# Kernel optimization log

Measured on AMD Instinct MI355X. Metric: run time of the kernel, lower is better.

The kernel has to match this reference:

```python
import jax, jax.numpy as jnp
import numpy as np
from jax.scipy.linalg import expm

DIM = 2048        # state dimension (init arg `dim`)
M_STEPS = 8192    # kernel length (init arg `timestamp`)
DELTA = 0.01      # ZOH step size (init arg `delta`)
STAB = 1e-3       # stabilizer added to A before inversion (matches torch code)


def setup_inputs() -> dict:
    key = jax.random.key(0)
    k1, k2, k3 = jax.random.split(key, 3)
    # Match the torch init scaling so matrix_exp/inv stay well-conditioned.
    A = jnp.eye(DIM, dtype=jnp.float32) * -0.01 \
        + jax.random.normal(k1, (DIM, DIM), dtype=jnp.float32) * 0.001
    B = jax.random.normal(k2, (DIM, 1), dtype=jnp.float32) * 0.01
    C = jax.random.normal(k3, (1, DIM), dtype=jnp.float32) * 0.01
    return {"A": A, "B": B, "C": C, "M": M_STEPS}


def reference(A, B, C, M):
    dim = A.shape[0]
    I = jnp.eye(dim, dtype=A.dtype)
    # --- ZOH discretization (torch._zoh_discretize) ---
    A_bar = expm(DELTA * A)                         # [dim, dim]
    A_inv = jnp.linalg.inv(A + STAB * I)            # [dim, dim]
    B_bar = A_inv @ (A_bar - I) @ (DELTA * B)       # [dim, 1]

    # --- kernel power iteration (torch._compute_K_bar) ---
    # K[t] = C @ A_bar^t @ B_bar. Since B_bar is a vector, the serial
    # matrix-power loop reduces to M sequential matvecs (same math).
    def step(x, _):
        term = (C @ x)[0, 0]        # scalar K_t
        return A_bar @ x, term      # advance state: A_bar^{t+1} B_bar

    _, terms = jax.lax.scan(step, B_bar, None, length=M)  # [M]
    K_bar = terms[::-1][None, :]    # flip along time, shape [1, M]
    return K_bar
```

## Files before the change

kernel.cpp:

```cpp
#include <hip/hip_runtime.h>
#include <hip/hip_bf16.h>


#define DIMN 2048
#define MSTEPS 8192
#define RSPLIT 91
#define NN ((size_t)DIMN * DIMN)
#define NBLK 32
#define ALD 36
#define GJP 65

typedef short short8 __attribute__((ext_vector_type(8)));
typedef float f32x4 __attribute__((ext_vector_type(4)));

__device__ inline void split1(float x, unsigned short& h, unsigned short& l)
{
  __hip_bfloat16 b = __float2bfloat16(x);
  h = *reinterpret_cast<unsigned short*>(&b);
  float r = x - __bfloat162float(b);
  __hip_bfloat16 b2 = __float2bfloat16(r);
  l = *reinterpret_cast<unsigned short*>(&b2);
}

__global__ __launch_bounds__(256)
void k_combine4(float* out,
                const float* i1, float c1, const float* i2, float c2,
                const float* i3, float c3, const float* i4, float c4,
                float dval)
{
  const int total = DIMN * DIMN;
  for (int idx = blockIdx.x * 256 + threadIdx.x; idx < total; idx += gridDim.x * 256) {
    float v = 0.f;
    if (i1) v = fmaf(c1, i1[idx], v);
    if (i2) v = fmaf(c2, i2[idx], v);
    if (i3) v = fmaf(c3, i3[idx], v);
    if (i4) v = fmaf(c4, i4[idx], v);
    if ((idx >> 11) == (idx & 2047)) v += dval;
    out[idx] = v;
  }
}

__global__ __launch_bounds__(256)
void k_fill64(const float* __restrict__ A, double* __restrict__ M)
{
  const int total = DIMN * DIMN;
  for (int idx = blockIdx.x * 256 + threadIdx.x; idx < total; idx += gridDim.x * 256) {
    double v = (double)A[idx];
    if ((idx >> 11) == (idx & 2047)) v += 1e-3;
    M[idx] = v;
  }
}

__global__ __launch_bounds__(256)
void k_split(const float* __restrict__ in, unsigned short* __restrict__ hi,
             unsigned short* __restrict__ lo)
{
  const int i4 = blockIdx.x * 256 + threadIdx.x;
  const float4 v = ((const float4*)in)[i4];
  ushort4 h, l;
  split1(v.x, h.x, l.x); split1(v.y, h.y, l.y);
  split1(v.z, h.z, l.z); split1(v.w, h.w, l.w);
  ((ushort4*)hi)[i4] = h;
  ((ushort4*)lo)[i4] = l;
}

__global__ __launch_bounds__(256)
void k_splitT(const float* __restrict__ in, unsigned short* __restrict__ hi,
              unsigned short* __restrict__ lo)
{
  __shared__ float t[32][33];
  const int bx = blockIdx.x * 32, by = blockIdx.y * 32;
  const int lx = threadIdx.x, ly = threadIdx.y;
  for (int dy = 0; dy < 32; dy += 8)
    t[ly + dy][lx] = in[(size_t)(by + ly + dy) * DIMN + bx + lx];
  __syncthreads();
  for (int dy = 0; dy < 32; dy += 8) {
    const size_t o = (size_t)(bx + ly + dy) * DIMN + by + lx;
    unsigned short h, l;
    split1(t[lx][ly + dy], h, l);
    hi[o] = h; lo[o] = l;
  }
}

__global__ __launch_bounds__(256)
void k_gemm3(const unsigned short* __restrict__ Ahg, const unsigned short* __restrict__ Alg,
             const unsigned short* __restrict__ Bhg, const unsigned short* __restrict__ Blg,
             float* __restrict__ C, float alpha,
             const float* E1, float c1, const float* E2, float c2)
{
  __shared__ unsigned short sAh[128 * ALD];
  __shared__ unsigned short sAl[128 * ALD];
  __shared__ unsigned short sBh[128 * ALD];
  __shared__ unsigned short sBl[128 * ALD];
  const int tid = threadIdx.x;
  const int wid = tid >> 6, lane = tid & 63;
  const int lr = lane & 15, lg = lane >> 4;
  const int wm = wid >> 1, wn = wid & 1;
  const int brow = blockIdx.y * 128, bcol = blockIdx.x * 128;
  const int sr = tid >> 1, sh = (tid & 1) * 16;

  const unsigned short* gAh = Ahg + (size_t)(brow + sr) * DIMN + sh;
  const unsigned short* gAl = Alg + (size_t)(brow + sr) * DIMN + sh;
  const unsigned short* gBh = Bhg + (size_t)(bcol + sr) * DIMN + sh;
  const unsigned short* gBl = Blg + (size_t)(bcol + sr) * DIMN + sh;

  f32x4 acc[4][4];
#pragma unroll
  for (int mf = 0; mf < 4; ++mf)
#pragma unroll
    for (int nf = 0; nf < 4; ++nf) acc[mf][nf] = (f32x4){0.f, 0.f, 0.f, 0.f};

  uint4 pa0 = *(const uint4*)gAh;      uint4 pa1 = *(const uint4*)(gAh + 8);
  uint4 pb0 = *(const uint4*)gAl;      uint4 pb1 = *(const uint4*)(gAl + 8);
  uint4 pc0 = *(const uint4*)gBh;      uint4 pc1 = *(const uint4*)(gBh + 8);
  uint4 pd0 = *(const uint4*)gBl;      uint4 pd1 = *(const uint4*)(gBl + 8);

  const int nk = DIMN / 32;
  for (int kt = 0; kt < nk; ++kt) {
    *(uint4*)&sAh[sr * ALD + sh] = pa0;  *(uint4*)&sAh[sr * ALD + sh + 8] = pa1;
    *(uint4*)&sAl[sr * ALD + sh] = pb0;  *(uint4*)&sAl[sr * ALD + sh + 8] = pb1;
    *(uint4*)&sBh[sr * ALD + sh] = pc0;  *(uint4*)&sBh[sr * ALD + sh + 8] = pc1;
    *(uint4*)&sBl[sr * ALD + sh] = pd0;  *(uint4*)&sBl[sr * ALD + sh + 8] = pd1;
    __syncthreads();
    if (kt + 1 < nk) {
      const int o = (kt + 1) * 32;
      pa0 = *(const uint4*)(gAh + o);  pa1 = *(const uint4*)(gAh + o + 8);
      pb0 = *(const uint4*)(gAl + o);  pb1 = *(const uint4*)(gAl + o + 8);
      pc0 = *(const uint4*)(gBh + o);  pc1 = *(const uint4*)(gBh + o + 8);
      pd0 = *(const uint4*)(gBl + o);  pd1 = *(const uint4*)(gBl + o + 8);
    }
    short8 bh[4], bl[4];
#pragma unroll
    for (int nf = 0; nf < 4; ++nf) {
      const int br = 64 * wn + 16 * nf + lr;
      bh[nf] = *(const short8*)&sBh[br * ALD + lg * 8];
      bl[nf] = *(const short8*)&sBl[br * ALD + lg * 8];
    }
#pragma unroll
    for (int mf = 0; mf < 4; ++mf) {
      const int ar = 64 * wm + 16 * mf + lr;
      const short8 ah = *(const short8*)&sAh[ar * ALD + lg * 8];
      const short8 al = *(const short8*)&sAl[ar * ALD + lg * 8];
#pragma unroll
      for (int nf = 0; nf < 4; ++nf) {
        acc[mf][nf] = __builtin_amdgcn_mfma_f32_16x16x32_bf16(ah, bh[nf], acc[mf][nf], 0, 0, 0);
        acc[mf][nf] = __builtin_amdgcn_mfma_f32_16x16x32_bf16(ah, bl[nf], acc[mf][nf], 0, 0, 0);
        acc[mf][nf] = __builtin_amdgcn_mfma_f32_16x16x32_bf16(al, bh[nf], acc[mf][nf], 0, 0, 0);
      }
    }
    __syncthreads();
  }
#pragma unroll
  for (int mf = 0; mf < 4; ++mf) {
#pragma unroll
    for (int nf = 0; nf < 4; ++nf) {
      const int col = bcol + 64 * wn + 16 * nf + lr;
#pragma unroll
      for (int i = 0; i < 4; ++i) {
        const int row = brow + 64 * wm + 16 * mf + 4 * lg + i;
        float v = alpha * acc[mf][nf][i];
        if (E1) v = fmaf(c1, E1[(size_t)row * DIMN + col], v);
        if (E2) v = fmaf(c2, E2[(size_t)row * DIMN + col], v);
        C[(size_t)row * DIMN + col] = v;
      }
    }
  }
}

#define DBM 64
#define DBK 8
__global__ __launch_bounds__(256)
void k_dgemm(const double* __restrict__ A, int lda,
             const double* __restrict__ B, int ldb,
             double* C, int ldc, int K, double alpha,
             const double* E1, int ld1, double c1)
{
  __shared__ double As[DBK][DBM];
  __shared__ double Bs[DBK][DBM];
  const int tid = threadIdx.x;
  const int tx = tid & 15, ty = tid >> 4;
  const int brow = blockIdx.y * DBM, bcol = blockIdx.x * DBM;

  const int arow = tid >> 2, ac0 = (tid & 3) * 2;
  const int brw  = tid >> 5, bc0 = (tid & 31) * 2;

  const double* Aptr = A + (size_t)(brow + arow) * lda + ac0;
  const double* Bptr = B + (size_t)brw * ldb + (bcol + bc0);

  double2 aPre = *(const double2*)Aptr;
  double2 bPre = *(const double2*)Bptr;

  double acc[4][4];
#pragma unroll
  for (int i = 0; i < 4; ++i)
#pragma unroll
    for (int j = 0; j < 4; ++j) acc[i][j] = 0.0;

  const int nk = K / DBK;
  for (int kt = 0; kt < nk; ++kt) {
    As[ac0 + 0][arow] = aPre.x;
    As[ac0 + 1][arow] = aPre.y;
    Bs[brw][bc0 + 0] = bPre.x;
    Bs[brw][bc0 + 1] = bPre.y;
    __syncthreads();
    if (kt + 1 < nk) {
      aPre = *(const double2*)(Aptr + (size_t)(kt + 1) * DBK);
      bPre = *(const double2*)(Bptr + (size_t)(kt + 1) * DBK * ldb);
    }
#pragma unroll
    for (int kk = 0; kk < DBK; ++kk) {
      double a[4], b[4];
#pragma unroll
      for (int i = 0; i < 4; ++i) a[i] = As[kk][ty * 4 + i];
#pragma unroll
      for (int j = 0; j < 4; ++j) b[j] = Bs[kk][tx * 4 + j];
#pragma unroll
      for (int i = 0; i < 4; ++i)
#pragma unroll
        for (int j = 0; j < 4; ++j)
          acc[i][j] = fma(a[i], b[j], acc[i][j]);
    }
    __syncthreads();
  }
#pragma unroll
  for (int i = 0; i < 4; ++i) {
    const int gi = brow + ty * 4 + i;
#pragma unroll
    for (int j = 0; j < 4; ++j) {
      const int gj = bcol + tx * 4 + j;
      double v = alpha * acc[i][j];
      if (E1) v = fma(c1, E1[(size_t)gi * ld1 + gj], v);
      C[(size_t)gi * ldc + gj] = v;
    }
  }
}

__global__ __launch_bounds__(256)
void k_gj64(const double* __restrict__ M, int ldm, double* __restrict__ W, int ldw)
{
  __shared__ double a[128][GJP];
  const int tid = threadIdx.x;
  const int rg = tid & 7;
  const int cg = tid >> 3;

  for (int idx = tid; idx < 64 * 64; idx += 256) {
    const int r = idx >> 6, c = idx & 63;
    a[c][r] = M[(size_t)r * ldm + c];
    a[64 + c][r] = (r == c) ? 1.0 : 0.0;
  }
  __syncthreads();

  for (int p = 0; p < 64; ++p) {
    const double rpv = 1.0 / a[p][p];
    const int c0 = p + 1 + cg;
    const int c1 = c0 + 32;
    const double prs0 = a[c0][p] * rpv;
    const double prs1 = a[c1][p] * rpv;
    double colp[8];
#pragma unroll
    for (int k = 0; k < 4; ++k) {
      const double2 t2 = *(const double2*)&a[p][rg * 8 + 2 * k];
      colp[2 * k] = t2.x; colp[2 * k + 1] = t2.y;
    }
    __syncthreads();
#pragma unroll
    for (int k = 0; k < 8; ++k) {
      const int r = rg * 8 + k;
      const bool isp = (r == p);
      const double v0 = a[c0][r];
      const double v1 = a[c1][r];
      a[c0][r] = isp ? prs0 : fma(-colp[k], prs0, v0);
      a[c1][r] = isp ? prs1 : fma(-colp[k], prs1, v1);
    }
    __syncthreads();
  }

  for (int idx = tid; idx < 64 * 64; idx += 256) {
    const int r = idx >> 6, c = idx & 63;
    W[(size_t)r * ldw + c] = a[64 + c][r];
  }
}

__global__ __launch_bounds__(256)
void k_stagefix(const double* __restrict__ Dinv, double* __restrict__ M,
                double* __restrict__ Rpan, double* __restrict__ Cpan, int p)
{
  const int blk = blockIdx.x;
  const int tid = threadIdx.x;
  if (blk >= 32) {
    const int idx = (blk - 32) * 256 + tid;
    const int i = idx >> 6, k = idx & 63;
    const bool inP = (i >> 6) == p;
    const size_t mo = (size_t)i * DIMN + p * 64 + k;
    double v = 0.0;
    if (!inP) { v = M[mo]; M[mo] = 0.0; }
    Cpan[idx] = v;
    return;
  }
  __shared__ double As[DBK][DBM];
  __shared__ double Bs[DBK][DBM];
  const double* Mrow = M + (size_t)p * 64 * DIMN;
  const int tx = tid & 15, ty = tid >> 4;
  const int bcol = blk * DBM;

  const int arow = tid >> 2, ac0 = (tid & 3) * 2;
  const int brw  = tid >> 5, bc0 = (tid & 31) * 2;

  const double* Aptr = Dinv + (size_t)arow * 64 + ac0;
  const double* Bptr = Mrow + (size_t)brw * DIMN + (bcol + bc0);

  double2 aPre = *(const double2*)Aptr;
  double2 bPre = *(const double2*)Bptr;

  double acc[4][4];
#pragma unroll
  for (int i = 0; i < 4; ++i)
#pragma unroll
    for (int j = 0; j < 4; ++j) acc[i][j] = 0.0;

  for (int kt = 0; kt < 8; ++kt) {
    As[ac0 + 0][arow] = aPre.x;
    As[ac0 + 1][arow] = aPre.y;
    Bs[brw][bc0 + 0] = bPre.x;
    Bs[brw][bc0 + 1] = bPre.y;
    __syncthreads();
    if (kt + 1 < 8) {
      aPre = *(const double2*)(Aptr + (size_t)(kt + 1) * DBK);
      bPre = *(const double2*)(Bptr + (size_t)(kt + 1) * DBK * DIMN);
    }
#pragma unroll
    for (int kk = 0; kk < DBK; ++kk) {
      double a[4], b[4];
#pragma unroll
      for (int i = 0; i < 4; ++i) a[i] = As[kk][ty * 4 + i];
#pragma unroll
      for (int j = 0; j < 4; ++j) b[j] = Bs[kk][tx * 4 + j];
#pragma unroll
      for (int i = 0; i < 4; ++i)
#pragma unroll
        for (int j = 0; j < 4; ++j)
          acc[i][j] = fma(a[i], b[j], acc[i][j]);
    }
    __syncthreads();
  }
  const bool pivcol = (bcol >> 6) == p;
#pragma unroll
  for (int i = 0; i < 4; ++i) {
    const int gi = ty * 4 + i;
#pragma unroll
    for (int j = 0; j < 4; ++j) {
      const int gj = bcol + tx * 4 + j;
      double v = pivcol ? Dinv[(size_t)gi * 64 + (gj & 63)] : acc[i][j];
      Rpan[(size_t)gi * DIMN + gj] = v;
      M[(size_t)(p * 64 + gi) * DIMN + gj] = v;
    }
  }
}

__global__ __launch_bounds__(256)
void k_mv(const float* __restrict__ Mat, const double* __restrict__ vin,
          double* vout, const double* vadd, double alpha)
{
  const int lane = threadIdx.x & 63;
  const int row = blockIdx.x * 4 + (threadIdx.x >> 6);
  const float* mrow = Mat + (size_t)row * DIMN;
  double acc = 0.0;
  for (int p = 0; p < DIMN; p += 256) {
    const float4 m = *(const float4*)&mrow[p + lane * 4];
    const double* vp = &vin[p + lane * 4];
    acc += (double)m.x * vp[0] + (double)m.y * vp[1] + (double)m.z * vp[2] + (double)m.w * vp[3];
  }
  for (int off = 32; off; off >>= 1) acc += __shfl_down(acc, off);
  if (lane == 0) vout[row] = alpha * acc + (vadd ? vadd[row] : 0.0);
}

__global__ __launch_bounds__(256)
void k_mv64(const double* __restrict__ W, const double* __restrict__ vin,
            double* vout, const double* vadd, double alpha)
{
  const int lane = threadIdx.x & 63;
  const int row = blockIdx.x * 4 + (threadIdx.x >> 6);
  const double* mrow = W + (size_t)row * DIMN;
  double acc = 0.0;
  for (int p = 0; p < DIMN; p += 256) {
    const int idx = p + lane * 4;
    const double2 m0 = *(const double2*)&mrow[idx];
    const double2 m1 = *(const double2*)&mrow[idx + 2];
    acc += m0.x * vin[idx] + m0.y * vin[idx + 1] + m1.x * vin[idx + 2] + m1.y * vin[idx + 3];
  }
  for (int off = 32; off; off >>= 1) acc += __shfl_down(acc, off);
  if (lane == 0) vout[row] = alpha * acc + (vadd ? vadd[row] : 0.0);
}

__global__ __launch_bounds__(256)
void k_mvres(const float* __restrict__ A, const double* __restrict__ x,
             const double* __restrict__ y, double* r)
{
  const int lane = threadIdx.x & 63;
  const int row = blockIdx.x * 4 + (threadIdx.x >> 6);
  const float* mrow = A + (size_t)row * DIMN;
  double acc = 0.0;
  for (int p = 0; p < DIMN; p += 256) {
    const float4 m = *(const float4*)&mrow[p + lane * 4];
    const double* vp = &x[p + lane * 4];
    acc += (double)m.x * vp[0] + (double)m.y * vp[1] + (double)m.z * vp[2] + (double)m.w * vp[3];
  }
  for (int off = 32; off; off >>= 1) acc += __shfl_down(acc, off);
  if (lane == 0) r[row] = y[row] - acc - 1e-3 * x[row];
}

__global__ __launch_bounds__(256)
void k_transpose(const float* __restrict__ in, float* __restrict__ out)
{
  __shared__ float t[32][33];
  const int bx = blockIdx.x * 32, by = blockIdx.y * 32;
  const int lx = threadIdx.x, ly = threadIdx.y;
  for (int dy = 0; dy < 32; dy += 8)
    t[ly + dy][lx] = in[(size_t)(by + ly + dy) * DIMN + bx + lx];
  __syncthreads();
  for (int dy = 0; dy < 32; dy += 8)
    out[(size_t)(bx + ly + dy) * DIMN + by + lx] = t[lx][ly + dy];
}

__global__ __launch_bounds__(256)
void k_chain(const float* __restrict__ E, const float* __restrict__ vin, float* __restrict__ vout,
             const float* __restrict__ ERT, const float* __restrict__ uin, float* __restrict__ uout)
{
  const int lane = threadIdx.x & 63;
  const int w = threadIdx.x >> 6;
  const int b = blockIdx.x;
  const float* mrow; const float* xin; float* xout; int row;
  if (b < 512) { row = b * 4 + w; mrow = E + (size_t)row * DIMN; xin = vin; xout = vout; }
  else { row = (b - 512) * 4 + w; mrow = ERT + (size_t)row * DIMN; xin = uin; xout = uout; }
  float acc = 0.f;
  for (int p = 0; p < DIMN; p += 256) {
    const float4 m = *(const float4*)&mrow[p + lane * 4];
    const float* vp = &xin[p + lane * 4];
    acc = fmaf(m.x, vp[0], acc);
    acc = fmaf(m.y, vp[1], acc);
    acc = fmaf(m.z, vp[2], acc);
    acc = fmaf(m.w, vp[3], acc);
  }
  for (int off = 32; off; off >>= 1) acc += __shfl_down(acc, off);
  if (lane == 0) xout[row] = xin[row] + acc;
}

__global__ __launch_bounds__(256)
void k_chainb(const float* __restrict__ E8, const float* __restrict__ Vin,
              float* __restrict__ Vout, int do_v,
              const float* __restrict__ A4T, const float* __restrict__ Uin,
              float* __restrict__ Uout)
{
  const int lane = threadIdx.x & 63;
  const int w = threadIdx.x >> 6;
  const int b = blockIdx.x;
  if (b < 512) {
    if (!do_v) return;
    const int row = b * 4 + w;
    const float* mrow = E8 + (size_t)row * DIMN;
    float acc[8];
#pragma unroll
    for (int r = 0; r < 8; ++r) acc[r] = 0.f;
    for (int p = 0; p < DIMN; p += 256) {
      const float4 m = *(const float4*)&mrow[p + lane * 4];
#pragma unroll
      for (int r = 0; r < 8; ++r) {
        const float4 v = *(const float4*)&Vin[(size_t)r * DIMN + p + lane * 4];
        acc[r] = fmaf(m.x, v.x, acc[r]);
        acc[r] = fmaf(m.y, v.y, acc[r]);
        acc[r] = fmaf(m.z, v.z, acc[r]);
        acc[r] = fmaf(m.w, v.w, acc[r]);
      }
    }
#pragma unroll
    for (int r = 0; r < 8; ++r) {
      float a = acc[r];
      for (int off = 32; off; off >>= 1) a += __shfl_down(a, off);
      if (lane == 0) Vout[(size_t)r * DIMN + row] = Vin[(size_t)r * DIMN + row] + a;
    }
  } else {
    const int row = (b - 512) * 4 + w;
    const float* mrow = A4T + (size_t)row * DIMN;
    float acc[4];
#pragma unroll
    for (int r = 0; r < 4; ++r) acc[r] = 0.f;
    for (int p = 0; p < DIMN; p += 256) {
      const float4 m = *(const float4*)&mrow[p + lane * 4];
#pragma unroll
      for (int r = 0; r < 4; ++r) {
        const float4 v = *(const float4*)&Uin[(size_t)r * DIMN + p + lane * 4];
        acc[r] = fmaf(m.x, v.x, acc[r]);
        acc[r] = fmaf(m.y, v.y, acc[r]);
        acc[r] = fmaf(m.z, v.z, acc[r]);
        acc[r] = fmaf(m.w, v.w, acc[r]);
      }
    }
#pragma unroll
    for (int r = 0; r < 4; ++r) {
      float a = acc[r];
      for (int off = 32; off; off >>= 1) a += __shfl_down(a, off);
      if (lane == 0) Uout[(size_t)r * DIMN + row] = Uin[(size_t)r * DIMN + row] + a;
    }
  }
}

__global__ __launch_bounds__(256)
void k_terms(const float* __restrict__ U, const float* __restrict__ V, float* __restrict__ out)
{
  const int lane = threadIdx.x & 63;
  const int t = blockIdx.x * 4 + (threadIdx.x >> 6);
  const int j = t / RSPLIT, i = t - j * RSPLIT;
  const float* u = U + (size_t)j * DIMN;
  const float* v = V + (size_t)i * DIMN;
  float acc = 0.f;
  for (int p = 0; p < DIMN; p += 256) {
    const float4 a4 = *(const float4*)&u[p + lane * 4];
    const float4 b4 = *(const float4*)&v[p + lane * 4];
    acc = fmaf(a4.x, b4.x, acc); acc = fmaf(a4.y, b4.y, acc);
    acc = fmaf(a4.z, b4.z, acc); acc = fmaf(a4.w, b4.w, acc);
  }
  for (int off = 32; off; off >>= 1) acc += __shfl_down(acc, off);
  if (lane == 0) out[MSTEPS - 1 - t] = acc;
}

__global__ void k_vecinit(const float* __restrict__ B, double* __restrict__ b64,
                          const float* __restrict__ Cv, float* __restrict__ U0)
{
  const int i = blockIdx.x * 256 + threadIdx.x;
  if (i < DIMN) { b64[i] = 0.01 * (double)B[i]; U0[i] = Cv[i]; }
}
__global__ void k_v0(const double* __restrict__ x64, float* __restrict__ V0)
{
  const int i = blockIdx.x * 256 + threadIdx.x;
  if (i < DIMN) V0[i] = (float)x64[i];
}

extern "C" void kernel_launch(void* const* d_in, const int* in_sizes, int n_in,
                              void* d_out, int out_size, void* d_ws, size_t ws_size,
                              hipStream_t stream)
{
  const float* dA = (const float*)d_in[0];
  const float* dB = (const float*)d_in[1];
  const float* dC = (const float*)d_in[2];
  float* out = (float*)d_out;

  float* fb = (float*)d_ws;
  float* Ebuf = fb;
  float* t1 = fb + NN;
  float* t2 = t1 + NN;
  float* t3 = t2 + NN;
  float* t4 = t3 + NN;
  float* t5 = t4 + NN;
  double* M64 = (double*)t1;
  double* scr64 = (double*)(fb + 6 * NN);
  double* Dinv = scr64;
  double* Cpan = Dinv + 64 * 64;
  double* Rpan = Cpan + (size_t)DIMN * 64;
  double* y64 = Rpan + (size_t)DIMN * 64;
  double* x64 = y64 + DIMN;
  double* r64 = x64 + DIMN;
  double* b64 = r64 + DIMN;
  float* V  = (float*)(b64 + DIMN);
  float* Uc = V + (size_t)96 * DIMN;

  const size_t needed = 6 * NN * 4
                        + (64 * 64 + 2 * (size_t)DIMN * 64 + 4 * (size_t)DIMN) * 8
                        + (size_t)(96 + 92) * DIMN * 4;
  if (ws_size < needed) return;

  const float* NUL = nullptr;
  dim3 cb(256), cg(2048);

  unsigned short* Ah  = (unsigned short*)t4;   unsigned short* Al  = Ah + NN;
  unsigned short* Ath = (unsigned short*)Ebuf; unsigned short* Atl = Ath + NN;
  unsigned short* Y2h = (unsigned short*)t1;   unsigned short* Y2l = Y2h + NN;
  unsigned short* Hth = (unsigned short*)t2;   unsigned short* Htl = Hth + NN;

  k_split<<<dim3(4096), cb, 0, stream>>>(dA, Ah, Al);
  k_splitT<<<dim3(64, 64), dim3(32, 8), 0, stream>>>(dA, Ath, Atl);
  k_gemm3<<<dim3(16, 16), cb, 0, stream>>>(Ah, Al, Ath, Atl, t3, 0.8281f,
                                           NUL, 0.f, NUL, 0.f);
  k_combine4<<<cg, cb, 0, stream>>>(Ebuf, t3, (float)(5e-5 / 0.8281), dA, 0.01f,
                                    NUL, 0, NUL, 0, 0.f);

  k_fill64<<<cg, cb, 0, stream>>>(dA, M64);
  for (int p = 0; p < NBLK; ++p) {
    double* Mrow = M64 + (size_t)p * 64 * DIMN;
    k_gj64<<<dim3(1), cb, 0, stream>>>(Mrow + p * 64, DIMN, Dinv, 64);
    k_stagefix<<<dim3(544), cb, 0, stream>>>(Dinv, M64, Rpan, Cpan, p);
    k_dgemm<<<dim3(32, 32), cb, 0, stream>>>(Cpan, 64, Rpan, DIMN, M64, DIMN, 64, -1.0,
                                             M64, DIMN, 1.0);
  }

  k_vecinit<<<dim3(8), cb, 0, stream>>>(dB, b64, dC, Uc);
  k_mv<<<dim3(512), cb, 0, stream>>>(Ebuf, b64, y64, (const double*)nullptr, 1.0);
  k_mv64<<<dim3(512), cb, 0, stream>>>(M64, y64, x64, (const double*)nullptr, 1.0);
  k_mvres<<<dim3(512), cb, 0, stream>>>(dA, x64, y64, r64);
  k_mv64<<<dim3(512), cb, 0, stream>>>(M64, r64, x64, x64, 1.0);
  k_v0<<<dim3(8), cb, 0, stream>>>(x64, V);

  k_combine4<<<cg, cb, 0, stream>>>(t4, dA, 0.91f / 6.f, t3, 1.f / 24.f,
                                    NUL, 0, NUL, 0, 0.f);
  k_split<<<dim3(4096), cb, 0, stream>>>(t3, Y2h, Y2l);
  k_splitT<<<dim3(64, 64), dim3(32, 8), 0, stream>>>(t4, Hth, Htl);
  k_gemm3<<<dim3(16, 16), cb, 0, stream>>>(Y2h, Y2l, Hth, Htl, t4, 1.f,
                                           t3, 0.5f, dA, 0.91f);
  k_transpose<<<dim3(64, 64), dim3(32, 8), 0, stream>>>(t4, t5);
  k_combine4<<<cg, cb, 0, stream>>>(t4, dA, 3.64f / 6.f, t3, 16.f / 24.f,
                                    NUL, 0, NUL, 0, 0.f);
  k_splitT<<<dim3(64, 64), dim3(32, 8), 0, stream>>>(t4, Hth, Htl);
  k_gemm3<<<dim3(16, 16), cb, 0, stream>>>(Y2h, Y2l, Hth, Htl, t4, 16.f,
                                           t3, 8.f, dA, 3.64f);
  k_combine4<<<cg, cb, 0, stream>>>(t1, dA, 0.08f, t3, (float)(0.0032 / 0.8281),
                                    NUL, 0, NUL, 0, 0.f);
  k_transpose<<<dim3(64, 64), dim3(32, 8), 0, stream>>>(t4, t3);

  for (int s = 0; s < 7; ++s) {
    k_chain<<<dim3(1024), cb, 0, stream>>>(Ebuf, V + (size_t)s * DIMN, V + (size_t)(s + 1) * DIMN,
                                           t5, Uc + (size_t)s * DIMN, Uc + (size_t)(s + 1) * DIMN);
  }
  for (int i = 0; i < 22; ++i) {
    k_chainb<<<dim3(1024), cb, 0, stream>>>(
        t1, V + (size_t)(8 * i) * DIMN, V + (size_t)(8 * i + 8) * DIMN, (i < 11) ? 1 : 0,
        t3, Uc + (size_t)(4 * i) * DIMN, Uc + (size_t)(4 * i + 4) * DIMN);
  }
  k_terms<<<dim3(2048), cb, 0, stream>>>(Uc, V, out);
}
```

Baseline: 4.229 ms.

## Fuse split/transpose kernels, retile the FP64 trailing update, swizzle GEMM block order

Merges the row and transposed bf16 hi/lo split of A into one kernel, and folds the combine step that builds the Horner operand into the transposed split, which removes several full-matrix passes over global memory. Replaces the 64x64 FP64 trailing-update GEMM in the blocked Gauss-Jordan inverse with a specialized 128x128 tile, 8x8-per-thread kernel that subtracts in place. Also remaps block indices in both GEMMs for better L2 locality. The larger FP64 tile uses only 256 blocks and many registers, which could reduce occupancy on the 32 sequential trailing updates.

Measured after the change: 4.425 ms. +4.6%, slower.

```diff
diff --git a/kernel.cpp b/kernel.cpp
--- a/kernel.cpp
+++ b/kernel.cpp
@@ -9,6 +9,7 @@
 #define NBLK 32
 #define ALD 36
 #define GJP 65
+#define TBM 128
 
 typedef short short8 __attribute__((ext_vector_type(8)));
 typedef float f32x4 __attribute__((ext_vector_type(4)));
@@ -65,20 +66,48 @@
 }
 
 __global__ __launch_bounds__(256)
-void k_splitT(const float* __restrict__ in, unsigned short* __restrict__ hi,
-              unsigned short* __restrict__ lo)
+void k_splitboth(const float* __restrict__ in,
+                 unsigned short* __restrict__ hi, unsigned short* __restrict__ lo,
+                 unsigned short* __restrict__ hiT, unsigned short* __restrict__ loT)
 {
   __shared__ float t[32][33];
   const int bx = blockIdx.x * 32, by = blockIdx.y * 32;
   const int lx = threadIdx.x, ly = threadIdx.y;
-  for (int dy = 0; dy < 32; dy += 8)
-    t[ly + dy][lx] = in[(size_t)(by + ly + dy) * DIMN + bx + lx];
+  for (int dy = 0; dy < 32; dy += 8) {
+    const size_t o = (size_t)(by + ly + dy) * DIMN + bx + lx;
+    const float v = in[o];
+    t[ly + dy][lx] = v;
+    unsigned short h, l;
+    split1(v, h, l);
+    hi[o] = h; lo[o] = l;
+  }
   __syncthreads();
   for (int dy = 0; dy < 32; dy += 8) {
     const size_t o = (size_t)(bx + ly + dy) * DIMN + by + lx;
     unsigned short h, l;
     split1(t[lx][ly + dy], h, l);
-    hi[o] = h; lo[o] = l;
+    hiT[o] = h; loT[o] = l;
+  }
+}
+
+__global__ __launch_bounds__(256)
+void k_combsplitT(const float* __restrict__ i1, float c1,
+                  const float* __restrict__ i2, float c2,
+                  unsigned short* __restrict__ hiT, unsigned short* __restrict__ loT)
+{
+  __shared__ float t[32][33];
+  const int bx = blockIdx.x * 32, by = blockIdx.y * 32;
+  const int lx = threadIdx.x, ly = threadIdx.y;
+  for (int dy = 0; dy < 32; dy += 8) {
+    const size_t o = (size_t)(by + ly + dy) * DIMN + bx + lx;
+    t[ly + dy][lx] = fmaf(c1, i1[o], c2 * i2[o]);
+  }
+  __syncthreads();
+  for (int dy = 0; dy < 32; dy += 8) {
+    const size_t o = (size_t)(bx + ly + dy) * DIMN + by + lx;
+    unsigned short h, l;
+    split1(t[lx][ly + dy], h, l);
+    hiT[o] = h; loT[o] = l;
   }
 }
 
@@ -96,7 +125,9 @@
   const int wid = tid >> 6, lane = tid & 63;
   const int lr = lane & 15, lg = lane >> 4;
   const int wm = wid >> 1, wn = wid & 1;
-  const int brow = blockIdx.y * 128, bcol = blockIdx.x * 128;
+  const int bid0 = blockIdx.y * 16 + blockIdx.x;
+  const int bids = (bid0 & 7) * 32 + (bid0 >> 3);
+  const int brow = (bids >> 4) * 128, bcol = (bids & 15) * 128;
   const int sr = tid >> 1, sh = (tid & 1) * 16;
 
   const unsigned short* gAh = Ahg + (size_t)(brow + sr) * DIMN + sh;
@@ -167,71 +198,66 @@
   }
 }
 
-#define DBM 64
-#define DBK 8
-__global__ __launch_bounds__(256)
-void k_dgemm(const double* __restrict__ A, int lda,
-             const double* __restrict__ B, int ldb,
-             double* C, int ldc, int K, double alpha,
-             const double* E1, int ld1, double c1)
-{
-  __shared__ double As[DBK][DBM];
-  __shared__ double Bs[DBK][DBM];
+__global__ __launch_bounds__(256, 1)
+void k_dtrail(const double* __restrict__ Cp, const double* __restrict__ Rp,
+              double* __restrict__ M)
+{
+  __shared__ double As[8][TBM];
+  __shared__ double Bs[8][TBM];
   const int tid = threadIdx.x;
+  const int bid0 = blockIdx.y * 16 + blockIdx.x;
+  const int bids = (bid0 & 7) * 32 + (bid0 >> 3);
+  const int brow = (bids >> 4) * TBM, bcol = (bids & 15) * TBM;
   const int tx = tid & 15, ty = tid >> 4;
-  const int brow = blockIdx.y * DBM, bcol = blockIdx.x * DBM;
-
-  const int arow = tid >> 2, ac0 = (tid & 3) * 2;
-  const int brw  = tid >> 5, bc0 = (tid & 31) * 2;
-
-  const double* Aptr = A + (size_t)(brow + arow) * lda + ac0;
-  const double* Bptr = B + (size_t)brw * ldb + (bcol + bc0);
-
-  double2 aPre = *(const double2*)Aptr;
-  double2 bPre = *(const double2*)Bptr;
-
-  double acc[4][4];
-#pragma unroll
-  for (int i = 0; i < 4; ++i)
-#pragma unroll
-    for (int j = 0; j < 4; ++j) acc[i][j] = 0.0;
-
-  const int nk = K / DBK;
-  for (int kt = 0; kt < nk; ++kt) {
-    As[ac0 + 0][arow] = aPre.x;
-    As[ac0 + 1][arow] = aPre.y;
-    Bs[brw][bc0 + 0] = bPre.x;
-    Bs[brw][bc0 + 1] = bPre.y;
-    __syncthreads();
-    if (kt + 1 < nk) {
-      aPre = *(const double2*)(Aptr + (size_t)(kt + 1) * DBK);
-      bPre = *(const double2*)(Bptr + (size_t)(kt + 1) * DBK * ldb);
-    }
-#pragma unroll
-    for (int kk = 0; kk < DBK; ++kk) {
-      double a[4], b[4];
-#pragma unroll
-      for (int i = 0; i < 4; ++i) a[i] = As[kk][ty * 4 + i];
-#pragma unroll
-      for (int j = 0; j < 4; ++j) b[j] = Bs[kk][tx * 4 + j];
-#pragma unroll
-      for (int i = 0; i < 4; ++i)
-#pragma unroll
-        for (int j = 0; j < 4; ++j)
+
+  const int ar = tid >> 1, ac = (tid & 1) * 4;
+  const int br = tid >> 5, bc = (tid & 31) * 4;
+
+  const double* Ap = Cp + (size_t)(brow + ar) * 64 + ac;
+  const double* Bp = Rp + (size_t)br * DIMN + (bcol + bc);
+
+  double4 aPre = *(const double4*)Ap;
+  double4 bPre = *(const double4*)Bp;
+
+  double acc[8][8];
+#pragma unroll
+  for (int i = 0; i < 8; ++i)
+#pragma unroll
+    for (int j = 0; j < 8; ++j) acc[i][j] = 0.0;
+
+  for (int kt = 0; kt < 8; ++kt) {
+    As[ac + 0][ar] = aPre.x; As[ac + 1][ar] = aPre.y;
+    As[ac + 2][ar] = aPre.z; As[ac + 3][ar] = aPre.w;
+    *(double4*)&Bs[br][bc] = bPre;
+    __syncthreads();
+    if (kt + 1 < 8) {
+      aPre = *(const double4*)(Ap + (kt + 1) * 8);
+      bPre = *(const double4*)(Bp + (size_t)(kt + 1) * 8 * DIMN);
+    }
+#pragma unroll
+    for (int kk = 0; kk < 8; ++kk) {
+      double a[8], b[8];
+#pragma unroll
+      for (int i = 0; i < 8; ++i) a[i] = As[kk][ty * 8 + i];
+#pragma unroll
+      for (int j = 0; j < 8; ++j) b[j] = Bs[kk][tx * 8 + j];
+#pragma unroll
+      for (int i = 0; i < 8; ++i)
+#pragma unroll
+        for (int j = 0; j < 8; ++j)
           acc[i][j] = fma(a[i], b[j], acc[i][j]);
     }
     __syncthreads();
   }
 #pragma unroll
-  for (int i = 0; i < 4; ++i) {
-    const int gi = brow + ty * 4 + i;
-#pragma unroll
-    for (int j = 0; j < 4; ++j) {
-      const int gj = bcol + tx * 4 + j;
-      double v = alpha * acc[i][j];
-      if (E1) v = fma(c1, E1[(size_t)gi * ld1 + gj], v);
-      C[(size_t)gi * ldc + gj] = v;
-    }
+  for (int i = 0; i < 8; ++i) {
+    const size_t ro = (size_t)(brow + ty * 8 + i) * DIMN + bcol + tx * 8;
+    double4 m0 = *(const double4*)&M[ro];
+    double4 m1 = *(const double4*)&M[ro + 4];
+    m0.x -= acc[i][0]; m0.y -= acc[i][1]; m0.z -= acc[i][2]; m0.w -= acc[i][3];
+    m1.x -= acc[i][4]; m1.y -= acc[i][5]; m1.z -= acc[i][6]; m1.w -= acc[i][7];
+    *(double4*)&M[ro] = m0;
+    *(double4*)&M[ro + 4] = m1;
   }
 }
 
@@ -281,6 +307,8 @@
   }
 }
 
+#define DBM 64
+#define DBK 8
 __global__ __launch_bounds__(256)
 void k_stagefix(const double* __restrict__ Dinv, double* __restrict__ M,
                 double* __restrict__ Rpan, double* __restrict__ Cpan, int p)
@@ -576,8 +604,7 @@
   unsigned short* Y2h = (unsigned short*)t1;   unsigned short* Y2l = Y2h + NN;
   unsigned short* Hth = (unsigned short*)t2;   unsigned short* Htl = Hth + NN;
 
-  k_split<<<dim3(4096), cb, 0, stream>>>(dA, Ah, Al);
-  k_splitT<<<dim3(64, 64), dim3(32, 8), 0, stream>>>(dA, Ath, Atl);
+  k_splitboth<<<dim3(64, 64), dim3(32, 8), 0, stream>>>(dA, Ah, Al, Ath, Atl);
   k_gemm3<<<dim3(16, 16), cb, 0, stream>>>(Ah, Al, Ath, Atl, t3, 0.8281f,
                                            NUL, 0.f, NUL, 0.f);
   k_combine4<<<cg, cb, 0, stream>>>(Ebuf, t3, (float)(5e-5 / 0.8281), dA, 0.01f,
@@ -588,8 +615,7 @@
     double* Mrow = M64 + (size_t)p * 64 * DIMN;
     k_gj64<<<dim3(1), cb, 0, stream>>>(Mrow + p * 64, DIMN, Dinv, 64);
     k_stagefix<<<dim3(544), cb, 0, stream>>>(Dinv, M64, Rpan, Cpan, p);
-    k_dgemm<<<dim3(32, 32), cb, 0, stream>>>(Cpan, 64, Rpan, DIMN, M64, DIMN, 64, -1.0,
-                                             M64, DIMN, 1.0);
+    k_dtrail<<<dim3(16, 16), cb, 0, stream>>>(Cpan, Rpan, M64);
   }
 
   k_vecinit<<<dim3(8), cb, 0, stream>>>(dB, b64, dC, Uc);
@@ -599,16 +625,14 @@
   k_mv64<<<dim3(512), cb, 0, stream>>>(M64, r64, x64, x64, 1.0);
   k_v0<<<dim3(8), cb, 0, stream>>>(x64, V);
 
-  k_combine4<<<cg, cb, 0, stream>>>(t4, dA, 0.91f / 6.f, t3, 1.f / 24.f,
-                                    NUL, 0, NUL, 0, 0.f);
   k_split<<<dim3(4096), cb, 0, stream>>>(t3, Y2h, Y2l);
-  k_splitT<<<dim3(64, 64), dim3(32, 8), 0, stream>>>(t4, Hth, Htl);
+  k_combsplitT<<<dim3(64, 64), dim3(32, 8), 0, stream>>>(dA, 0.91f / 6.f,
+                                                         t3, 1.f / 24.f, Hth, Htl);
   k_gemm3<<<dim3(16, 16), cb, 0, stream>>>(Y2h, Y2l, Hth, Htl, t4, 1.f,
                                            t3, 0.5f, dA, 0.91f);
   k_transpose<<<dim3(64, 64), dim3(32, 8), 0, stream>>>(t4, t5);
-  k_combine4<<<cg, cb, 0, stream>>>(t4, dA, 3.64f / 6.f, t3, 16.f / 24.f,
-                                    NUL, 0, NUL, 0, 0.f);
-  k_splitT<<<dim3(64, 64), dim3(32, 8), 0, stream>>>(t4, Hth, Htl);
+  k_combsplitT<<<dim3(64, 64), dim3(32, 8), 0, stream>>>(dA, 3.64f / 6.f,
+                                                         t3, 16.f / 24.f, Hth, Htl);
   k_gemm3<<<dim3(16, 16), cb, 0, stream>>>(Y2h, Y2l, Hth, Htl, t4, 16.f,
                                            t3, 8.f, dA, 3.64f);
   k_combine4<<<cg, cb, 0, stream>>>(t1, dA, 0.08f, t3, (float)(0.0032 / 0.8281),
```
